# Optimization experiments

Measured on AMD Instinct MI355X. Metric: run time of the kernel, lower is better.

The kernel has to match this reference:

```python
import jax, jax.numpy as jnp
import numpy as np

N_NODES = 50000
N_EDGES = 800000


def _deg_inv_sqrt(idx, n):
    deg = jax.ops.segment_sum(jnp.ones(idx.shape[0], jnp.float32), idx, num_segments=n)
    return jnp.power(jnp.clip(deg, 1.0, None), -0.5)


def _gcn_layer(x, W, b, src, dst, out_norm, in_norm, n):
    # left degree norm, dense matmul, gather-scatter-sum over edges, right norm, bias
    h = (x * out_norm[:, None]) @ W
    agg = jax.ops.segment_sum(h[src], dst, num_segments=n)
    return agg * in_norm[:, None] + b


def setup_inputs() -> dict:
    key = jax.random.key(0)
    ks = jax.random.split(key, 8)
    def xavier(k, fi, fo):
        a = np.sqrt(6.0 / (fi + fo))
        return jax.random.uniform(k, (fi, fo), jnp.float32, -a, a)
    x = jax.random.normal(ks[0], (N_NODES, 256), jnp.float32)
    edge_index = jax.random.randint(ks[1], (2, N_EDGES), 0, N_NODES, dtype=jnp.int64)
    return {
        "x": x,
        "edge_index": edge_index,
        "W0": xavier(ks[2], 256, 128), "b0": jnp.zeros((128,), jnp.float32),
        "W1": xavier(ks[3], 128, 128), "b1": jnp.zeros((128,), jnp.float32),
        "W2": xavier(ks[4], 128, 128), "b2": jnp.zeros((128,), jnp.float32),
        "W3": xavier(ks[5], 128, 64),  "b3": jnp.zeros((64,), jnp.float32),
    }


def reference(x, edge_index, W0, b0, W1, b1, W2, b2, W3, b3):
    n = x.shape[0]
    src, dst = edge_index[0], edge_index[1]
    out_norm = _deg_inv_sqrt(src, n)  # out-degree based (src side)
    in_norm = _deg_inv_sqrt(dst, n)   # in-degree based (dst side)
    Ws = [W0, W1, W2, W3]
    bs = [b0, b1, b2, b3]
    h = x
    for i in range(4):
        h = _gcn_layer(h, Ws[i], bs[i], src, dst, out_norm, in_norm, n)
        if i < 3:  # relu on all but final layer
            h = jax.nn.relu(h)
    return h
```

## Files before the change

kernel.cpp:

```cpp
#include <hip/hip_runtime.h>
#include <hip/hip_fp16.h>


typedef __attribute__((ext_vector_type(8))) short short8;
typedef __attribute__((ext_vector_type(4))) float f32x4;

#define NRANGE 8
#define NCHUNK 64
#define RMAX   6272

__device__ inline unsigned short bf16_rne(float v) {
    union { float f; unsigned u; } c; c.f = v;
    unsigned u = c.u;
    unsigned lsb = (u >> 16) & 1u;
    u += 0x7fffu + lsb;
    return (unsigned short)(u >> 16);
}
__device__ inline float bf16_to_f(unsigned short h) {
    union { unsigned u; float f; } c; c.u = ((unsigned)h) << 16;
    return c.f;
}
__device__ inline void split_bf16(float v, unsigned short& hi, unsigned short& lo) {
    hi = bf16_rne(v);
    lo = bf16_rne(v - bf16_to_f(hi));
}


__global__ __launch_bounds__(256) void k_hist(const int* __restrict__ src,
                                              const int* __restrict__ dst,
                                              int ne, int R, int E,
                                              int* __restrict__ cnt_s,
                                              int* __restrict__ cnt_d,
                                              int* __restrict__ pos) {
    __shared__ int hs[RMAX];
    __shared__ int hd[RMAX];
    int r = blockIdx.x & (NRANGE - 1);
    int c = blockIdx.x >> 3;
    int tid = threadIdx.x;
    for (int i = tid; i < R; i += 256) { hs[i] = 0; hd[i] = 0; }
    __syncthreads();
    int lo = r * R, hi = lo + R;
    int e0 = c * E, e1 = min(e0 + E, ne);
    for (int i = e0 + tid; i < e1; i += 256) {
        int s = src[i], d = dst[i];
        if (s >= lo && s < hi) atomicAdd(&hs[s - lo], 1);
        if (d >= lo && d < hi) {
            int p = atomicAdd(&hd[d - lo], 1);
            pos[i] = p;
        }
    }
    __syncthreads();
    int base = (r * NCHUNK + c) * R;
    for (int i = tid; i < R; i += 256) {
        cnt_s[base + i] = hs[i];
        cnt_d[base + i] = hd[i];
    }
}

__global__ void k_reduce_norms(const int* __restrict__ cnt_s,
                               const int* __restrict__ cnt_d, int R, int n,
                               float* __restrict__ onrm, float* __restrict__ inrm,
                               int* __restrict__ degd_sum) {
    int i = blockIdx.x * blockDim.x + threadIdx.x;
    if (i >= NRANGE * R) return;
    int r = i / R, ip = i - r * R;
    int ds = 0, dd = 0;
    for (int c = 0; c < NCHUNK; ++c) {
        ds += cnt_s[(r * NCHUNK + c) * R + ip];
        dd += cnt_d[(r * NCHUNK + c) * R + ip];
    }
    degd_sum[i] = dd;
    if (i < n) {
        onrm[i] = rsqrtf((float)max(ds, 1));
        inrm[i] = rsqrtf((float)max(dd, 1));
    }
}

__global__ __launch_bounds__(1024) void k_scan(const int* __restrict__ deg, int n,
                                               int* __restrict__ row_ptr) {
    __shared__ int wsum[16];
    __shared__ int carry;
    int tid = threadIdx.x;
    int lane = tid & 63;
    int wid = tid >> 6;
    if (tid == 0) carry = 0;
    __syncthreads();
    int n4 = (n + 3) >> 2;
    for (int base = 0; base < n4; base += 1024) {
        int i4 = base + tid;
        int4 v = make_int4(0, 0, 0, 0);
        if (i4 < n4) v = ((const int4*)deg)[i4];
        int s = v.x + v.y + v.z + v.w;
        int x = s;
#pragma unroll
        for (int off = 1; off < 64; off <<= 1) {
            int y = __shfl_up(x, off, 64);
            if (lane >= off) x += y;
        }
        if (lane == 63) wsum[wid] = x;
        __syncthreads();
        if (wid == 0 && lane < 16) {
            int w = wsum[lane];
#pragma unroll
            for (int off = 1; off < 16; off <<= 1) {
                int y = __shfl_up(w, off, 16);
                if (lane >= off) w += y;
            }
            wsum[lane] = w;
        }
        __syncthreads();
        int excl = x - s + carry + (wid > 0 ? wsum[wid - 1] : 0);
        if (i4 < n4) {
            int e0 = excl, e1 = e0 + v.x, e2 = e1 + v.y, e3 = e2 + v.z;
            ((int4*)row_ptr)[i4] = make_int4(e0, e1, e2, e3);
        }
        __syncthreads();
        if (tid == 0) carry += wsum[15];
        __syncthreads();
    }
    if (tid == 0) row_ptr[n] = carry;
}

__global__ void k_cursors(const int* __restrict__ row_ptr,
                          const int* __restrict__ cnt_d, int R, int n,
                          int* __restrict__ cbase) {
    int i = blockIdx.x * blockDim.x + threadIdx.x;
    if (i >= NRANGE * R) return;
    int r = i / R, ip = i - r * R;
    int run = (i < n) ? row_ptr[i] : 0;
    for (int c = 0; c < NCHUNK; ++c) {
        int idx = (r * NCHUNK + c) * R + ip;
        cbase[idx] = run;
        run += cnt_d[idx];
    }
}

__global__ void k_csr_scatter(const int* __restrict__ src,
                              const int* __restrict__ dst,
                              const int* __restrict__ pos,
                              const int* __restrict__ cbase,
                              int ne, int R, int E,
                              int* __restrict__ eidx) {
    int i = blockIdx.x * blockDim.x + threadIdx.x;
    if (i >= ne) return;
    int d = dst[i];
    int r = d / R, ip = d - r * R;
    int c = i / E;
    eidx[cbase[(r * NCHUNK + c) * R + ip] + pos[i]] = src[i];
}


__global__ void k_split_w_all(const float* __restrict__ W0, const float* __restrict__ W1,
                              const float* __restrict__ W2, const float* __restrict__ W3,
                              unsigned short* __restrict__ Wh0, unsigned short* __restrict__ Wl0,
                              unsigned short* __restrict__ Wh1, unsigned short* __restrict__ Wl1,
                              unsigned short* __restrict__ Wh2, unsigned short* __restrict__ Wl2,
                              unsigned short* __restrict__ Wh3, unsigned short* __restrict__ Wl3) {
    int i = blockIdx.x * blockDim.x + threadIdx.x;
    const float* W; unsigned short *Wh, *Wl; int K, F, off;
    if (i < 32768)                    { W = W0; Wh = Wh0; Wl = Wl0; K = 256; F = 128; off = i; }
    else if (i < 32768 + 16384)       { W = W1; Wh = Wh1; Wl = Wl1; K = 128; F = 128; off = i - 32768; }
    else if (i < 32768 + 32768)       { W = W2; Wh = Wh2; Wl = Wl2; K = 128; F = 128; off = i - 49152; }
    else if (i < 32768 + 32768 + 8192){ W = W3; Wh = Wh3; Wl = Wl3; K = 128; F = 64;  off = i - 65536; }
    else return;
    int k = off / F, c = off % F;
    unsigned short h, l;
    split_bf16(W[k * F + c], h, l);
    Wh[c * K + k] = h;
    Wl[c * K + k] = l;
}

template <int K, int N, bool FA>
__global__ __launch_bounds__(256) void k_mm(const unsigned short* __restrict__ Ah,
                                            const unsigned short* __restrict__ Al,
                                            const float* __restrict__ Xf,
                                            const float* __restrict__ onrm,
                                            const unsigned short* __restrict__ Bh,
                                            const unsigned short* __restrict__ Bl,
                                            __half* __restrict__ H, int n) {
    constexpr int KT = 128;
    constexpr int NT = N / 16;
    constexpr int NKT = K / KT;
    __shared__ unsigned short sBh[N * KT];
    __shared__ unsigned short sBl[N * KT];

    int tid = threadIdx.x;
    int w = tid >> 6, lane = tid & 63;
    int quad = lane >> 4, l16 = lane & 15;
    int row_base = blockIdx.x * 128 + w * 32;

    int ar0 = row_base + l16;
    int ar1 = row_base + 16 + l16;
    if (ar0 >= n) ar0 = n - 1;
    if (ar1 >= n) ar1 = n - 1;

    float on0 = 0.f, on1 = 0.f;
    if (FA) { on0 = onrm[ar0]; on1 = onrm[ar1]; }

    f32x4 acc[2][NT];
#pragma unroll
    for (int m = 0; m < 2; ++m)
#pragma unroll
        for (int t = 0; t < NT; ++t) acc[m][t] = (f32x4){0.f, 0.f, 0.f, 0.f};

    for (int kt = 0; kt < NKT; ++kt) {
        if (kt) __syncthreads();
        for (int idx = tid; idx < N * 16; idx += 256) {
            int c = idx >> 4;
            int g = idx & 15;
            short8 vh = *(const short8*)(Bh + (size_t)c * K + kt * KT + g * 8);
            short8 vl = *(const short8*)(Bl + (size_t)c * K + kt * KT + g * 8);
            int sg = g ^ (c & 15);
            *(short8*)(&sBh[c * KT + sg * 8]) = vh;
            *(short8*)(&sBl[c * KT + sg * 8]) = vl;
        }
        __syncthreads();

#pragma unroll
        for (int k0 = 0; k0 < KT; k0 += 32) {
            int eoff = k0 + quad * 8;
            short8 a0hv, a0lv, a1hv, a1lv;
            if (FA) {
                const float* x0 = Xf + (size_t)ar0 * K + kt * KT + eoff;
                const float* x1 = Xf + (size_t)ar1 * K + kt * KT + eoff;
                float4 p00 = *(const float4*)x0;
                float4 p01 = *(const float4*)(x0 + 4);
                float4 p10 = *(const float4*)x1;
                float4 p11 = *(const float4*)(x1 + 4);
                float e0[8] = {p00.x, p00.y, p00.z, p00.w, p01.x, p01.y, p01.z, p01.w};
                float e1[8] = {p10.x, p10.y, p10.z, p10.w, p11.x, p11.y, p11.z, p11.w};
#pragma unroll
                for (int q = 0; q < 8; ++q) {
                    unsigned short hh, ll;
                    split_bf16(e0[q] * on0, hh, ll);
                    a0hv[q] = (short)hh; a0lv[q] = (short)ll;
                    split_bf16(e1[q] * on1, hh, ll);
                    a1hv[q] = (short)hh; a1lv[q] = (short)ll;
                }
            } else {
                a0hv = *(const short8*)(Ah + (size_t)ar0 * K + kt * KT + eoff);
                a0lv = *(const short8*)(Al + (size_t)ar0 * K + kt * KT + eoff);
                a1hv = *(const short8*)(Ah + (size_t)ar1 * K + kt * KT + eoff);
                a1lv = *(const short8*)(Al + (size_t)ar1 * K + kt * KT + eoff);
            }
            int g = (k0 >> 3) + quad;
            int sg8 = (g ^ l16) * 8;
#pragma unroll
            for (int t = 0; t < NT; ++t) {
                int cb = (t * 16 + l16) * KT;
                short8 bh = *(const short8*)(&sBh[cb + sg8]);
                short8 bl = *(const short8*)(&sBl[cb + sg8]);
                acc[0][t] = __builtin_amdgcn_mfma_f32_16x16x32_bf16(a0hv, bh, acc[0][t], 0, 0, 0);
                acc[0][t] = __builtin_amdgcn_mfma_f32_16x16x32_bf16(a0lv, bh, acc[0][t], 0, 0, 0);
                acc[0][t] = __builtin_amdgcn_mfma_f32_16x16x32_bf16(a0hv, bl, acc[0][t], 0, 0, 0);
                acc[1][t] = __builtin_amdgcn_mfma_f32_16x16x32_bf16(a1hv, bh, acc[1][t], 0, 0, 0);
                acc[1][t] = __builtin_amdgcn_mfma_f32_16x16x32_bf16(a1lv, bh, acc[1][t], 0, 0, 0);
                acc[1][t] = __builtin_amdgcn_mfma_f32_16x16x32_bf16(a1hv, bl, acc[1][t], 0, 0, 0);
            }
        }
    }

#pragma unroll
    for (int m = 0; m < 2; ++m) {
#pragma unroll
        for (int t = 0; t < NT; ++t) {
#pragma unroll
            for (int r = 0; r < 4; ++r) {
                int grow = row_base + m * 16 + quad * 4 + r;
                if (grow < n) H[(size_t)grow * N + t * 16 + l16] = __float2half(acc[m][t][r]);
            }
        }
    }
}


__global__ __launch_bounds__(256) void k_agg128_split(const __half* __restrict__ h,
                                                      const int* __restrict__ row_ptr,
                                                      const int* __restrict__ eidx,
                                                      const float* __restrict__ inrm,
                                                      const float* __restrict__ onrm,
                                                      const float* __restrict__ bias,
                                                      unsigned short* __restrict__ Ah,
                                                      unsigned short* __restrict__ Al, int n) {
    int wave = threadIdx.x >> 6;
    int lane = threadIdx.x & 63;
    int g = lane >> 4;
    int l = lane & 15;
    int node = blockIdx.x * 16 + wave * 4 + g;
    bool valid = node < n;
    int nd = valid ? node : n - 1;
    int beg = row_ptr[nd], end = row_ptr[nd + 1];
    const short8* h8 = (const short8*)h;

    float a[4][8];
#pragma unroll
    for (int u = 0; u < 4; ++u)
#pragma unroll
        for (int c = 0; c < 8; ++c) a[u][c] = 0.f;

    int j = beg;
    for (; j + 4 <= end; j += 4) {
        int s[4];
#pragma unroll
        for (int u = 0; u < 4; ++u) s[u] = eidx[j + u];
        short8 v[4];
#pragma unroll
        for (int u = 0; u < 4; ++u) v[u] = h8[(size_t)s[u] * 16 + l];
#pragma unroll
        for (int u = 0; u < 4; ++u) {
            const __half2* ph = reinterpret_cast<const __half2*>(&v[u]);
#pragma unroll
            for (int p = 0; p < 4; ++p) {
                float2 f = __half22float2(ph[p]);
                a[u][2 * p] += f.x;
                a[u][2 * p + 1] += f.y;
            }
        }
    }
    for (; j < end; ++j) {
        short8 v = h8[(size_t)eidx[j] * 16 + l];
        const __half2* ph = reinterpret_cast<const __half2*>(&v);
#pragma unroll
        for (int p = 0; p < 4; ++p) {
            float2 f = __half22float2(ph[p]);
            a[0][2 * p] += f.x;
            a[0][2 * p + 1] += f.y;
        }
    }

    float nrm = inrm[nd];
    float on = onrm[nd];
    float4 b0 = ((const float4*)bias)[l * 2];
    float4 b1 = ((const float4*)bias)[l * 2 + 1];
    float bb[8] = {b0.x, b0.y, b0.z, b0.w, b1.x, b1.y, b1.z, b1.w};
    short8 hv, lv;
#pragma unroll
    for (int c = 0; c < 8; ++c) {
        float s = (a[0][c] + a[1][c]) + (a[2][c] + a[3][c]);
        float o = fmaxf(s * nrm + bb[c], 0.f) * on;
        unsigned short hh, ll;
        split_bf16(o, hh, ll);
        hv[c] = (short)hh;
        lv[c] = (short)ll;
    }
    if (valid) {
        ((short8*)Ah)[(size_t)node * 16 + l] = hv;
        ((short8*)Al)[(size_t)node * 16 + l] = lv;
    }
}

__global__ __launch_bounds__(256) void k_agg64(const __half* __restrict__ h,
                                               const int* __restrict__ row_ptr,
                                               const int* __restrict__ eidx,
                                               const float* __restrict__ inrm,
                                               const float* __restrict__ bias,
                                               float* __restrict__ out, int n) {
    int wave = threadIdx.x >> 6;
    int lane = threadIdx.x & 63;
    int g = lane >> 4;
    int l = lane & 15;
    int node = blockIdx.x * 16 + wave * 4 + g;
    bool valid = node < n;
    int nd = valid ? node : n - 1;
    int beg = row_ptr[nd], end = row_ptr[nd + 1];
    const ushort4* h4 = (const ushort4*)h;

    float a[8][4];
#pragma unroll
    for (int u = 0; u < 8; ++u)
#pragma unroll
        for (int c = 0; c < 4; ++c) a[u][c] = 0.f;

    int j = beg;
    for (; j + 8 <= end; j += 8) {
        int s[8];
#pragma unroll
        for (int u = 0; u < 8; ++u) s[u] = eidx[j + u];
        ushort4 v[8];
#pragma unroll
        for (int u = 0; u < 8; ++u) v[u] = h4[(size_t)s[u] * 16 + l];
#pragma unroll
        for (int u = 0; u < 8; ++u) {
            const __half2* ph = reinterpret_cast<const __half2*>(&v[u]);
            float2 f0 = __half22float2(ph[0]);
            float2 f1 = __half22float2(ph[1]);
            a[u][0] += f0.x; a[u][1] += f0.y; a[u][2] += f1.x; a[u][3] += f1.y;
        }
    }
    for (; j < end; ++j) {
        ushort4 v = h4[(size_t)eidx[j] * 16 + l];
        const __half2* ph = reinterpret_cast<const __half2*>(&v);
        float2 f0 = __half22float2(ph[0]);
        float2 f1 = __half22float2(ph[1]);
        a[0][0] += f0.x; a[0][1] += f0.y; a[0][2] += f1.x; a[0][3] += f1.y;
    }

    float nrm = inrm[nd];
    float4 b4 = ((const float4*)bias)[l];
    float4 o;
    float s0 = ((a[0][0] + a[1][0]) + (a[2][0] + a[3][0])) + ((a[4][0] + a[5][0]) + (a[6][0] + a[7][0]));
    float s1 = ((a[0][1] + a[1][1]) + (a[2][1] + a[3][1])) + ((a[4][1] + a[5][1]) + (a[6][1] + a[7][1]));
    float s2 = ((a[0][2] + a[1][2]) + (a[2][2] + a[3][2])) + ((a[4][2] + a[5][2]) + (a[6][2] + a[7][2]));
    float s3 = ((a[0][3] + a[1][3]) + (a[2][3] + a[3][3])) + ((a[4][3] + a[5][3]) + (a[6][3] + a[7][3]));
    o.x = s0 * nrm + b4.x;
    o.y = s1 * nrm + b4.y;
    o.z = s2 * nrm + b4.z;
    o.w = s3 * nrm + b4.w;
    if (valid) ((float4*)out)[(size_t)node * 16 + l] = o;
}

template <int K, int FO, int TX, int TY, int RPT>
__global__ __launch_bounds__(256) void k_matmul(const float* __restrict__ X,
                                                const float* __restrict__ W,
                                                const float* __restrict__ onrm,
                                                float* __restrict__ H, int n) {
    constexpr int BROWS = TY * RPT;
    constexpr int LDK = K + 1;
    __shared__ float xs[BROWS * LDK];
    int tx = threadIdx.x, ty = threadIdx.y;
    int tid = ty * TX + tx;
    int row0 = blockIdx.x * BROWS;

    for (int idx = tid; idx < BROWS * K; idx += 256) {
        int r = idx / K;
        int k = idx - r * K;
        int row = row0 + r;
        xs[r * LDK + k] = (row < n) ? X[(size_t)row * K + k] : 0.f;
    }
    __syncthreads();

    float4 acc[RPT];
#pragma unroll
    for (int r = 0; r < RPT; ++r) acc[r] = make_float4(0.f, 0.f, 0.f, 0.f);

    const float4* W4 = (const float4*)W;
#pragma unroll 4
    for (int k = 0; k < K; ++k) {
        float4 w = W4[k * (FO / 4) + tx];
#pragma unroll
        for (int r = 0; r < RPT; ++r) {
            float xv = xs[(ty * RPT + r) * LDK + k];
            acc[r].x += xv * w.x;
            acc[r].y += xv * w.y;
            acc[r].z += xv * w.z;
            acc[r].w += xv * w.w;
        }
    }

#pragma unroll
    for (int r = 0; r < RPT; ++r) {
        int row = row0 + ty * RPT + r;
        if (row < n) {
            float s = onrm[row];
            float4 o = make_float4(acc[r].x * s, acc[r].y * s, acc[r].z * s, acc[r].w * s);
            ((float4*)H)[(size_t)row * (FO / 4) + tx] = o;
        }
    }
}

__global__ __launch_bounds__(256) void k_agg128f(const float* __restrict__ h,
                                                 const int* __restrict__ row_ptr,
                                                 const int* __restrict__ eidx,
                                                 const float* __restrict__ inrm,
                                                 const float* __restrict__ bias,
                                                 float* __restrict__ out, int n, int relu) {
    int node = blockIdx.x * 4 + (threadIdx.x >> 6);
    int lane = threadIdx.x & 63;
    if (node >= n) return;
    int beg = row_ptr[node], end = row_ptr[node + 1];
    const float2* h2 = (const float2*)h;
    float ax = 0.f, ay = 0.f;
    for (int j = beg; j < end; ++j) {
        int s = eidx[j];
        float2 v = h2[(size_t)s * 64 + lane];
        ax += v.x;
        ay += v.y;
    }
    float nrm = inrm[node];
    float2 b2 = ((const float2*)bias)[lane];
    float ox = ax * nrm + b2.x;
    float oy = ay * nrm + b2.y;
    if (relu) { ox = fmaxf(ox, 0.f); oy = fmaxf(oy, 0.f); }
    float2 o; o.x = ox; o.y = oy;
    ((float2*)out)[(size_t)node * 64 + lane] = o;
}

__global__ __launch_bounds__(256) void k_agg64f(const float* __restrict__ h,
                                                const int* __restrict__ row_ptr,
                                                const int* __restrict__ eidx,
                                                const float* __restrict__ inrm,
                                                const float* __restrict__ bias,
                                                float* __restrict__ out, int n) {
    int node = blockIdx.x * 4 + (threadIdx.x >> 6);
    int lane = threadIdx.x & 63;
    if (node >= n) return;
    int beg = row_ptr[node], end = row_ptr[node + 1];
    float acc = 0.f;
    for (int j = beg; j < end; ++j) {
        int s = eidx[j];
        acc += h[(size_t)s * 64 + lane];
    }
    out[(size_t)node * 64 + lane] = acc * inrm[node] + bias[lane];
}

__global__ void k_degrees_leg(const int* __restrict__ src, const int* __restrict__ dst,
                              int ne, int* __restrict__ degs, int* __restrict__ degd) {
    int i = blockIdx.x * blockDim.x + threadIdx.x;
    if (i < ne) {
        atomicAdd(&degs[src[i]], 1);
        atomicAdd(&degd[dst[i]], 1);
    }
}
__global__ void k_norms_leg(const int* __restrict__ degs, const int* __restrict__ degd,
                            float* __restrict__ onrm, float* __restrict__ inrm,
                            int* __restrict__ degd_sum, int n) {
    int i = blockIdx.x * blockDim.x + threadIdx.x;
    if (i < n) {
        degd_sum[i] = degd[i];
        onrm[i] = rsqrtf((float)max(degs[i], 1));
        inrm[i] = rsqrtf((float)max(degd[i], 1));
    }
}
__global__ void k_copy_int(const int* __restrict__ a, int* __restrict__ b, int n) {
    int i = blockIdx.x * blockDim.x + threadIdx.x;
    if (i < n) b[i] = a[i];
}
__global__ void k_build_csr_leg(const int* __restrict__ src, const int* __restrict__ dst,
                                int ne, int* __restrict__ cursor, int* __restrict__ eidx) {
    int i = blockIdx.x * blockDim.x + threadIdx.x;
    if (i < ne) {
        int p = atomicAdd(&cursor[dst[i]], 1);
        eidx[p] = src[i];
    }
}

static inline size_t align_up(size_t v, size_t a) { return (v + a - 1) & ~(a - 1); }

extern "C" void kernel_launch(void* const* d_in, const int* in_sizes, int n_in,
                              void* d_out, int out_size, void* d_ws, size_t ws_size,
                              hipStream_t stream) {
    const float* x  = (const float*)d_in[0];
    const int* ei   = (const int*)d_in[1];
    const float* W0 = (const float*)d_in[2];
    const float* b0 = (const float*)d_in[3];
    const float* W1 = (const float*)d_in[4];
    const float* b1 = (const float*)d_in[5];
    const float* W2 = (const float*)d_in[6];
    const float* b2 = (const float*)d_in[7];
    const float* W3 = (const float*)d_in[8];
    const float* b3 = (const float*)d_in[9];

    const int n  = in_sizes[0] / 256;
    const int ne = in_sizes[1] / 2;
    const int n_pad = (n + 127) & ~127;
    const int* src = ei;
    const int* dst = ei + ne;

    char* ws = (char*)d_ws;
    size_t off = 0;
    auto take = [&](size_t bytes) { void* p = ws + off; off = align_up(off + bytes, 256); return p; };
    int* row_ptr  = (int*)take((size_t)(n_pad + 4) * 4);
    int* degd_sum = (int*)take((size_t)n_pad * 4);
    int* eidx     = (int*)take((size_t)ne * 4);
    float* onrm   = (float*)take((size_t)n * 4);
    float* inrm   = (float*)take((size_t)n * 4);

    size_t off_save = off;
    unsigned short* Ah  = (unsigned short*)take((size_t)n_pad * 256 * 2);
    unsigned short* Al  = (unsigned short*)take((size_t)n_pad * 256 * 2);
    __half* hbuf        = (__half*)take((size_t)n * 128 * 2);
    unsigned short* Wh0 = (unsigned short*)take(256 * 128 * 2);
    unsigned short* Wl0 = (unsigned short*)take(256 * 128 * 2);
    unsigned short* Wh1 = (unsigned short*)take(128 * 128 * 2);
    unsigned short* Wl1 = (unsigned short*)take(128 * 128 * 2);
    unsigned short* Wh2 = (unsigned short*)take(128 * 128 * 2);
    unsigned short* Wl2 = (unsigned short*)take(128 * 128 * 2);
    unsigned short* Wh3 = (unsigned short*)take(128 * 64 * 2);
    unsigned short* Wl3 = (unsigned short*)take(128 * 64 * 2);
    bool use_mfma = (off <= ws_size);

    char* pre = (char*)Ah;
    const int R = ((n + NRANGE * 64 - 1) / (NRANGE * 64)) * 64;
    const size_t cntSz = align_up((size_t)NRANGE * NCHUNK * R * 4, 256);
    int* cnt_s = (int*)pre;
    int* cnt_d = (int*)(pre + cntSz);
    int* cbase = (int*)(pre + 2 * cntSz);
    int* pos   = (int*)(pre + 3 * cntSz);

    const int aggGrid = (n + 15) / 16;

    if (R <= RMAX) {
        const int E = (ne + NCHUNK - 1) / NCHUNK;
        k_hist<<<NRANGE * NCHUNK, 256, 0, stream>>>(src, dst, ne, R, E, cnt_s, cnt_d, pos);
        k_reduce_norms<<<(NRANGE * R + 255) / 256, 256, 0, stream>>>(cnt_s, cnt_d, R, n,
                                                                     onrm, inrm, degd_sum);
        k_scan<<<1, 1024, 0, stream>>>(degd_sum, n, row_ptr);
        k_cursors<<<(NRANGE * R + 255) / 256, 256, 0, stream>>>(row_ptr, cnt_d, R, n, cbase);
        k_csr_scatter<<<(ne + 255) / 256, 256, 0, stream>>>(src, dst, pos, cbase, ne, R, E, eidx);
    } else {
        int* degs   = cnt_s;
        int* degd   = cnt_s + n_pad;
        int* cursor = cnt_s + 2 * n_pad;
        hipMemsetAsync(degs, 0, (size_t)2 * n_pad * 4, stream);
        k_degrees_leg<<<(ne + 255) / 256, 256, 0, stream>>>(src, dst, ne, degs, degd);
        k_norms_leg<<<(n + 255) / 256, 256, 0, stream>>>(degs, degd, onrm, inrm, degd_sum, n);
        k_scan<<<1, 1024, 0, stream>>>(degd_sum, n, row_ptr);
        k_copy_int<<<(n + 255) / 256, 256, 0, stream>>>(row_ptr, cursor, n);
        k_build_csr_leg<<<(ne + 255) / 256, 256, 0, stream>>>(src, dst, ne, cursor, eidx);
    }

    if (use_mfma) {
        k_split_w_all<<<(73728 + 255) / 256, 256, 0, stream>>>(
            W0, W1, W2, W3, Wh0, Wl0, Wh1, Wl1, Wh2, Wl2, Wh3, Wl3);

        const int mmGrid = n_pad / 128;
        k_mm<256, 128, true><<<mmGrid, 256, 0, stream>>>(nullptr, nullptr, x, onrm, Wh0, Wl0, hbuf, n);
        k_agg128_split<<<aggGrid, 256, 0, stream>>>(hbuf, row_ptr, eidx, inrm, onrm, b0, Ah, Al, n);
        k_mm<128, 128, false><<<mmGrid, 256, 0, stream>>>(Ah, Al, nullptr, nullptr, Wh1, Wl1, hbuf, n);
        k_agg128_split<<<aggGrid, 256, 0, stream>>>(hbuf, row_ptr, eidx, inrm, onrm, b1, Ah, Al, n);
        k_mm<128, 128, false><<<mmGrid, 256, 0, stream>>>(Ah, Al, nullptr, nullptr, Wh2, Wl2, hbuf, n);
        k_agg128_split<<<aggGrid, 256, 0, stream>>>(hbuf, row_ptr, eidx, inrm, onrm, b2, Ah, Al, n);
        k_mm<128, 64, false><<<mmGrid, 256, 0, stream>>>(Ah, Al, nullptr, nullptr, Wh3, Wl3, hbuf, n);
        k_agg64<<<aggGrid, 256, 0, stream>>>(hbuf, row_ptr, eidx, inrm, b3, (float*)d_out, n);
    } else {
        off = off_save;
        float* hbufF  = (float*)take((size_t)n * 128 * 4);
        float* xnextF = (float*)take((size_t)n * 128 * 4);
        const int aggGridF = (n + 3) / 4;

        k_matmul<256, 128, 32, 8, 4><<<(n + 31) / 32, dim3(32, 8), 0, stream>>>(x, W0, onrm, hbufF, n);
        k_agg128f<<<aggGridF, 256, 0, stream>>>(hbufF, row_ptr, eidx, inrm, b0, xnextF, n, 1);
        k_matmul<128, 128, 32, 8, 4><<<(n + 31) / 32, dim3(32, 8), 0, stream>>>(xnextF, W1, onrm, hbufF, n);
        k_agg128f<<<aggGridF, 256, 0, stream>>>(hbufF, row_ptr, eidx, inrm, b1, xnextF, n, 1);
        k_matmul<128, 128, 32, 8, 4><<<(n + 31) / 32, dim3(32, 8), 0, stream>>>(xnextF, W2, onrm, hbufF, n);
        k_agg128f<<<aggGridF, 256, 0, stream>>>(hbufF, row_ptr, eidx, inrm, b2, xnextF, n, 1);
        k_matmul<128, 64, 16, 16, 4><<<(n + 63) / 64, dim3(16, 16), 0, stream>>>(xnextF, W3, onrm, hbufF, n);
        k_agg64f<<<aggGridF, 256, 0, stream>>>(hbufF, row_ptr, eidx, inrm, b3, (float*)d_out, n);
    }
}
```

Before: 356.1 us.

## Replace single-block scan with multi-block scan and fuse weight split into histogram

Swaps the single-block 1024-thread degree scan for a block-sum reduction folded into the norm kernel plus a multi-block cursor kernel that scans block sums and per-node degrees together. The weight bf16 hi/lo split is folded into extra blocks of the histogram kernel, removing a separate launch. This targets a serial single-block bottleneck and launch overhead during CSR construction. It adds a blocksum buffer in workspace and assumes no more than 256 scan blocks.

```diff
diff --git a/kernel.cpp b/kernel.cpp
--- a/kernel.cpp
+++ b/kernel.cpp
@@ -31,9 +31,32 @@
                                               int ne, int R, int E,
                                               int* __restrict__ cnt_s,
                                               int* __restrict__ cnt_d,
-                                              int* __restrict__ pos) {
+                                              int* __restrict__ pos,
+                                              const float* __restrict__ W0,
+                                              const float* __restrict__ W1,
+                                              const float* __restrict__ W2,
+                                              const float* __restrict__ W3,
+                                              unsigned short* __restrict__ Wh0, unsigned short* __restrict__ Wl0,
+                                              unsigned short* __restrict__ Wh1, unsigned short* __restrict__ Wl1,
+                                              unsigned short* __restrict__ Wh2, unsigned short* __restrict__ Wl2,
+                                              unsigned short* __restrict__ Wh3, unsigned short* __restrict__ Wl3) {
     __shared__ int hs[RMAX];
     __shared__ int hd[RMAX];
+    if (blockIdx.x >= NRANGE * NCHUNK) {
+        int i = (blockIdx.x - NRANGE * NCHUNK) * 256 + threadIdx.x;
+        const float* W; unsigned short *Wh, *Wl; int K, F, off;
+        if (i < 32768)                     { W = W0; Wh = Wh0; Wl = Wl0; K = 256; F = 128; off = i; }
+        else if (i < 32768 + 16384)        { W = W1; Wh = Wh1; Wl = Wl1; K = 128; F = 128; off = i - 32768; }
+        else if (i < 32768 + 32768)        { W = W2; Wh = Wh2; Wl = Wl2; K = 128; F = 128; off = i - 49152; }
+        else if (i < 32768 + 32768 + 8192) { W = W3; Wh = Wh3; Wl = Wl3; K = 128; F = 64;  off = i - 65536; }
+        else return;
+        int k = off / F, c = off % F;
+        unsigned short h, l;
+        split_bf16(W[k * F + c], h, l);
+        Wh[c * K + k] = h;
+        Wl[c * K + k] = l;
+        return;
+    }
     int r = blockIdx.x & (NRANGE - 1);
     int c = blockIdx.x >> 3;
     int tid = threadIdx.x;
@@ -57,12 +80,15 @@
     }
 }
 
-__global__ void k_reduce_norms(const int* __restrict__ cnt_s,
-                               const int* __restrict__ cnt_d, int R, int n,
-                               float* __restrict__ onrm, float* __restrict__ inrm,
-                               int* __restrict__ degd_sum) {
-    int i = blockIdx.x * blockDim.x + threadIdx.x;
-    if (i >= NRANGE * R) return;
+__global__ __launch_bounds__(256) void k_reduce_norms(const int* __restrict__ cnt_s,
+                                                      const int* __restrict__ cnt_d, int R, int n,
+                                                      float* __restrict__ onrm,
+                                                      float* __restrict__ inrm,
+                                                      int* __restrict__ degd_sum,
+                                                      int* __restrict__ blocksum) {
+    __shared__ int red[256];
+    int tid = threadIdx.x;
+    int i = blockIdx.x * 256 + tid;
     int r = i / R, ip = i - r * R;
     int ds = 0, dd = 0;
     for (int c = 0; c < NCHUNK; ++c) {
@@ -74,60 +100,55 @@
         onrm[i] = rsqrtf((float)max(ds, 1));
         inrm[i] = rsqrtf((float)max(dd, 1));
     }
-}
-
-__global__ __launch_bounds__(1024) void k_scan(const int* __restrict__ deg, int n,
-                                               int* __restrict__ row_ptr) {
-    __shared__ int wsum[16];
-    __shared__ int carry;
+    red[tid] = dd;
+    __syncthreads();
+#pragma unroll
+    for (int off = 128; off > 0; off >>= 1) {
+        if (tid < off) red[tid] += red[tid + off];
+        __syncthreads();
+    }
+    if (tid == 0) blocksum[blockIdx.x] = red[0];
+}
+
+__global__ __launch_bounds__(256) void k_cursors2(const int* __restrict__ blocksum, int nblk,
+                                                  const int* __restrict__ degd_sum,
+                                                  const int* __restrict__ cnt_d, int R,
+                                                  int* __restrict__ row_ptr,
+                                                  int* __restrict__ cbase, int total_i) {
+    __shared__ int bs[256];
+    __shared__ int wsum[4];
     int tid = threadIdx.x;
-    int lane = tid & 63;
-    int wid = tid >> 6;
-    if (tid == 0) carry = 0;
+    bs[tid] = (tid < nblk) ? blocksum[tid] : 0;
     __syncthreads();
-    int n4 = (n + 3) >> 2;
-    for (int base = 0; base < n4; base += 1024) {
-        int i4 = base + tid;
-        int4 v = make_int4(0, 0, 0, 0);
-        if (i4 < n4) v = ((const int4*)deg)[i4];
-        int s = v.x + v.y + v.z + v.w;
-        int x = s;
-#pragma unroll
-        for (int off = 1; off < 64; off <<= 1) {
-            int y = __shfl_up(x, off, 64);
-            if (lane >= off) x += y;
-        }
-        if (lane == 63) wsum[wid] = x;
+#pragma unroll
+    for (int off = 1; off < 256; off <<= 1) {
+        int v = bs[tid];
+        int u = (tid >= off) ? bs[tid - off] : 0;
         __syncthreads();
-        if (wid == 0 && lane < 16) {
-            int w = wsum[lane];
-#pragma unroll
-            for (int off = 1; off < 16; off <<= 1) {
-                int y = __shfl_up(w, off, 16);
-                if (lane >= off) w += y;
-            }
-            wsum[lane] = w;
-        }
+        bs[tid] = v + u;
         __syncthreads();
-        int excl = x - s + carry + (wid > 0 ? wsum[wid - 1] : 0);
-        if (i4 < n4) {
-            int e0 = excl, e1 = e0 + v.x, e2 = e1 + v.y, e3 = e2 + v.z;
-            ((int4*)row_ptr)[i4] = make_int4(e0, e1, e2, e3);
-        }
-        __syncthreads();
-        if (tid == 0) carry += wsum[15];
-        __syncthreads();
-    }
-    if (tid == 0) row_ptr[n] = carry;
-}
-
-__global__ void k_cursors(const int* __restrict__ row_ptr,
-                          const int* __restrict__ cnt_d, int R, int n,
-                          int* __restrict__ cbase) {
-    int i = blockIdx.x * blockDim.x + threadIdx.x;
-    if (i >= NRANGE * R) return;
+    }
+    int base = (blockIdx.x > 0) ? bs[blockIdx.x - 1] : 0;
+
+    int i = blockIdx.x * 256 + tid;
+    int dd = degd_sum[i];
+    int lane = tid & 63, wid = tid >> 6;
+    int x = dd;
+#pragma unroll
+    for (int off = 1; off < 64; off <<= 1) {
+        int y = __shfl_up(x, off, 64);
+        if (lane >= off) x += y;
+    }
+    if (lane == 63) wsum[wid] = x;
+    __syncthreads();
+    int wbase = 0;
+    for (int wp = 0; wp < wid; ++wp) wbase += wsum[wp];
+    int excl = base + wbase + (x - dd);
+    row_ptr[i] = excl;
+    if (i == total_i - 1) row_ptr[total_i] = excl + dd;
+
     int r = i / R, ip = i - r * R;
-    int run = (i < n) ? row_ptr[i] : 0;
+    int run = excl;
     for (int c = 0; c < NCHUNK; ++c) {
         int idx = (r * NCHUNK + c) * R + ip;
         cbase[idx] = run;
@@ -409,6 +430,51 @@
     if (valid) ((float4*)out)[(size_t)node * 16 + l] = o;
 }
 
+__global__ __launch_bounds__(1024) void k_scan(const int* __restrict__ deg, int n,
+                                               int* __restrict__ row_ptr) {
+    __shared__ int wsum[16];
+    __shared__ int carry;
+    int tid = threadIdx.x;
+    int lane = tid & 63;
+    int wid = tid >> 6;
+    if (tid == 0) carry = 0;
+    __syncthreads();
+    int n4 = (n + 3) >> 2;
+    for (int base = 0; base < n4; base += 1024) {
+        int i4 = base + tid;
+        int4 v = make_int4(0, 0, 0, 0);
+        if (i4 < n4) v = ((const int4*)deg)[i4];
+        int s = v.x + v.y + v.z + v.w;
+        int x = s;
+#pragma unroll
+        for (int off = 1; off < 64; off <<= 1) {
+            int y = __shfl_up(x, off, 64);
+            if (lane >= off) x += y;
+        }
+        if (lane == 63) wsum[wid] = x;
+        __syncthreads();
+        if (wid == 0 && lane < 16) {
+            int w = wsum[lane];
+#pragma unroll
+            for (int off = 1; off < 16; off <<= 1) {
+                int y = __shfl_up(w, off, 16);
+                if (lane >= off) w += y;
+            }
+            wsum[lane] = w;
+        }
+        __syncthreads();
+        int excl = x - s + carry + (wid > 0 ? wsum[wid - 1] : 0);
+        if (i4 < n4) {
+            int e0 = excl, e1 = e0 + v.x, e2 = e1 + v.y, e3 = e2 + v.z;
+            ((int4*)row_ptr)[i4] = make_int4(e0, e1, e2, e3);
+        }
+        __syncthreads();
+        if (tid == 0) carry += wsum[15];
+        __syncthreads();
+    }
+    if (tid == 0) row_ptr[n] = carry;
+}
+
 template <int K, int FO, int TX, int TY, int RPT>
 __global__ __launch_bounds__(256) void k_matmul(const float* __restrict__ X,
                                                 const float* __restrict__ W,
@@ -586,16 +652,22 @@
     int* cnt_d = (int*)(pre + cntSz);
     int* cbase = (int*)(pre + 2 * cntSz);
     int* pos   = (int*)(pre + 3 * cntSz);
+    int* blocksum = (int*)(pre + 3 * cntSz + align_up((size_t)ne * 4, 256));
 
     const int aggGrid = (n + 15) / 16;
 
     if (R <= RMAX) {
         const int E = (ne + NCHUNK - 1) / NCHUNK;
-        k_hist<<<NRANGE * NCHUNK, 256, 0, stream>>>(src, dst, ne, R, E, cnt_s, cnt_d, pos);
-        k_reduce_norms<<<(NRANGE * R + 255) / 256, 256, 0, stream>>>(cnt_s, cnt_d, R, n,
-                                                                     onrm, inrm, degd_sum);
-        k_scan<<<1, 1024, 0, stream>>>(degd_sum, n, row_ptr);
-        k_cursors<<<(NRANGE * R + 255) / 256, 256, 0, stream>>>(row_ptr, cnt_d, R, n, cbase);
+        const int nscan = NRANGE * R;
+        const int nblk = nscan / 256;
+        const int wsplitBlocks = use_mfma ? 288 : 0;
+        k_hist<<<NRANGE * NCHUNK + wsplitBlocks, 256, 0, stream>>>(
+            src, dst, ne, R, E, cnt_s, cnt_d, pos,
+            W0, W1, W2, W3, Wh0, Wl0, Wh1, Wl1, Wh2, Wl2, Wh3, Wl3);
+        k_reduce_norms<<<nblk, 256, 0, stream>>>(cnt_s, cnt_d, R, n,
+                                                 onrm, inrm, degd_sum, blocksum);
+        k_cursors2<<<nblk, 256, 0, stream>>>(blocksum, nblk, degd_sum, cnt_d, R,
+                                             row_ptr, cbase, nscan);
         k_csr_scatter<<<(ne + 255) / 256, 256, 0, stream>>>(src, dst, pos, cbase, ne, R, E, eidx);
     } else {
         int* degs   = cnt_s;
@@ -607,12 +679,12 @@
         k_scan<<<1, 1024, 0, stream>>>(degd_sum, n, row_ptr);
         k_copy_int<<<(n + 255) / 256, 256, 0, stream>>>(row_ptr, cursor, n);
         k_build_csr_leg<<<(ne + 255) / 256, 256, 0, stream>>>(src, dst, ne, cursor, eidx);
+        if (use_mfma)
+            k_split_w_all<<<(73728 + 255) / 256, 256, 0, stream>>>(
+                W0, W1, W2, W3, Wh0, Wl0, Wh1, Wl1, Wh2, Wl2, Wh3, Wl3);
     }
 
     if (use_mfma) {
-        k_split_w_all<<<(73728 + 255) / 256, 256, 0, stream>>>(
-            W0, W1, W2, W3, Wh0, Wl0, Wh1, Wl1, Wh2, Wl2, Wh3, Wl3);
-
         const int mmGrid = n_pad / 128;
         k_mm<256, 128, true><<<mmGrid, 256, 0, stream>>>(nullptr, nullptr, x, onrm, Wh0, Wl0, hbuf, n);
         k_agg128_split<<<aggGrid, 256, 0, stream>>>(hbuf, row_ptr, eidx, inrm, onrm, b0, Ah, Al, n);
```

After: 339.0 us. 4.8% less time.
